# Optimization experiments

Hardware: AMD Instinct MI355X
Metric: run time of the kernel (lower is better)

Reference implementation:

```python
import jax, jax.numpy as jnp
import numpy as np

# ---- static config (from init_kwargs) ----
B_, L_, DM = 4, 2048, 1024
EXPAND, HEADDIM, DSTATE, DCONV = 2, 64, 64, 7
DIN = EXPAND * DM            # 2048
NH = DIN // HEADDIM          # 32
CONV_DIM = DIN + 2 * DSTATE  # 2176 (x, B, C go through the depthwise conv)
DPROJ = 2 * DIN + 2 * DSTATE + 2 * NH  # 4288 (z, xBC, dt_fwd, dt_bwd)
EPS = 1e-5


def setup_inputs() -> dict:
    key = jax.random.key(0)
    ks = jax.random.split(key, 8)
    s = lambda d: 1.0 / np.sqrt(d)
    # dt_bias = inv_softplus(dt) with dt ~ logUniform(1e-3, 0.1)  (Mamba2/Hydra init)
    dt = jnp.exp(jax.random.uniform(ks[3], (NH,)) * (np.log(0.1) - np.log(0.001)) + np.log(0.001))
    return {
        "x": jax.random.normal(ks[0], (B_, L_, DM), jnp.float32),
        "ln_gamma": jnp.ones((DM,), jnp.float32),
        "ln_beta": jnp.zeros((DM,), jnp.float32),
        "W_in": jax.random.normal(ks[1], (DPROJ, DM), jnp.float32) * s(DM),
        "conv_w": jax.random.normal(ks[2], (CONV_DIM, DCONV), jnp.float32) * s(DCONV),
        "conv_b": jnp.zeros((CONV_DIM,), jnp.float32),
        "dt_bias": jnp.log(jnp.expm1(dt)),
        "A_log": jnp.log(jax.random.uniform(ks[4], (NH,), minval=1.0, maxval=16.0)),
        "fc_D_w": jax.random.normal(ks[5], (NH, DIN), jnp.float32) * s(DIN),
        "D": jnp.ones((NH,), jnp.float32),
        "norm_w": jnp.ones((DIN,), jnp.float32),
        "W_out": jax.random.normal(ks[6], (DM, DIN), jnp.float32) * s(DIN),
    }


def _hydra_layer(x, ln_gamma, ln_beta, W_in, conv_w, conv_b, dt_bias, A_log,
                 fc_D_w, D, norm_w, W_out):
    res = x
    # LayerNorm
    mu = jnp.mean(x, -1, keepdims=True)
    var = jnp.mean((x - mu) ** 2, -1, keepdims=True)
    u = (x - mu) * jax.lax.rsqrt(var + EPS) * ln_gamma + ln_beta

    # input projection -> z (gate), xBC (conv stream), dt (fwd+bwd)
    zxbcdt = jnp.einsum('bld,pd->blp', u, W_in)
    z = zxbcdt[..., :DIN]
    xBC = zxbcdt[..., DIN:DIN + CONV_DIM]
    dt = zxbcdt[..., DIN + CONV_DIM:]               # (B,L,2*NH)

    # depthwise 'same' conv along L + SiLU (bidirectional model -> symmetric pad)
    xBC_c = jax.lax.conv_general_dilated(
        xBC.transpose(0, 2, 1), conv_w[:, None, :], (1,),
        [(DCONV // 2, DCONV // 2)], feature_group_count=CONV_DIM)
    xBC = jax.nn.silu((xBC_c + conv_b[None, :, None]).transpose(0, 2, 1))

    xs = xBC[..., :DIN]                             # (B,L,DIN)
    Bm = xBC[..., DIN:DIN + DSTATE]                 # (B,L,N)
    Cm = xBC[..., DIN + DSTATE:]                    # (B,L,N)

    flip = lambda a: a[:, ::-1]
    # stack forward and (flipped) backward direction along batch
    dt2 = jax.nn.softplus(jnp.concatenate([dt[..., :NH], flip(dt[..., NH:])], 0) + dt_bias)  # (2B,L,NH)
    x2 = jnp.concatenate([xs, flip(xs)], 0).reshape(2 * B_, L_, NH, HEADDIM)
    B2 = jnp.concatenate([Bm, flip(Bm)], 0)
    C2 = jnp.concatenate([Cm, flip(Cm)], 0)

    A = -jnp.exp(A_log)                             # (NH,)
    dA = jnp.exp(dt2 * A)                           # (2B,L,NH)

    # selective SSM recurrence: h_t = dA_t * h_{t-1} + dt_t * x_t B_t^T ; y_t = h_t C_t
    def step(h, inp):
        dA_t, dt_t, B_t, C_t, x_t = inp
        dBx = (dt_t[:, :, None, None] * x_t[..., None]) * B_t[:, None, None, :]
        h = dA_t[:, :, None, None] * h + dBx        # (2B,NH,P,N)
        y = jnp.einsum('bhpn,bn->bhp', h, C_t)
        return h, y

    h0 = jnp.zeros((2 * B_, NH, HEADDIM, DSTATE), x.dtype)
    tr = lambda a: jnp.moveaxis(a, 1, 0)
    _, ys = jax.lax.scan(step, h0, (tr(dA), tr(dt2), tr(B2), tr(C2), tr(x2)))
    y = jnp.moveaxis(ys, 0, 1)                      # (2B,L,NH,P)

    # shift by one: strictly off-diagonal part of the quasiseparable mixing matrix
    y = jnp.concatenate([jnp.zeros_like(y[:, :1]), y[:, :-1]], axis=1)
    y = y[:B_] + flip(y[B_:])                       # (B,L,NH,P)

    # data-dependent diagonal: D(x) = fc_D(x) + D, applied per head
    Ddata = jnp.einsum('bld,hd->blh', xs, fc_D_w) + D
    y = y + xs.reshape(B_, L_, NH, HEADDIM) * Ddata[..., None]
    y = y.reshape(B_, L_, DIN)

    # gated RMSNorm (norm after gate)
    y = y * jax.nn.silu(z)
    y = y * jax.lax.rsqrt(jnp.mean(y * y, -1, keepdims=True) + EPS) * norm_w

    # out proj + residual (dropout is identity in eval)
    return res + jnp.einsum('bli,di->bld', y, W_out)


def reference(x, ln_gamma, ln_beta, W_in, conv_w, conv_b, dt_bias, A_log,
              fc_D_w, D, norm_w, W_out):
    return _hydra_layer(x, ln_gamma, ln_beta, W_in, conv_w, conv_b, dt_bias,
                        A_log, fc_D_w, D, norm_w, W_out)
```

## Files before the change

### kernel.cpp

```cpp
#include <hip/hip_runtime.h>
#include <stdint.h>

#define B_   4
#define L_   2048
#define DM   1024
#define DIN  2048
#define NH   32
#define HD   64
#define DSTATE 64
#define DCONV  7
#define CONV_DIM 2176
#define DPROJ 4288
#define NPAD 4352
#define BL   8192
#define EPS  1e-5f
#define QC   128
#define NCH  16

typedef unsigned short u16;
typedef unsigned int   u32;
typedef __bf16 bf16x8 __attribute__((ext_vector_type(8)));
typedef float  f32x4  __attribute__((ext_vector_type(4)));

__device__ __forceinline__ float b2f(u32 b) { return __uint_as_float(b << 16); }
__device__ __forceinline__ u16 f2b(float f) {
    u32 u = __float_as_uint(f);
    u32 r = (u + 0x7fffu + ((u >> 16) & 1u)) >> 16;
    return (u16)r;
}
__device__ __forceinline__ void unpack8(uint4 v, float* f) {
    f[0] = b2f(v.x & 0xffffu); f[1] = b2f(v.x >> 16);
    f[2] = b2f(v.y & 0xffffu); f[3] = b2f(v.y >> 16);
    f[4] = b2f(v.z & 0xffffu); f[5] = b2f(v.z >> 16);
    f[6] = b2f(v.w & 0xffffu); f[7] = b2f(v.w >> 16);
}
__device__ __forceinline__ uint4 pack8(const float* f) {
    uint4 v;
    v.x = (u32)f2b(f[0]) | ((u32)f2b(f[1]) << 16);
    v.y = (u32)f2b(f[2]) | ((u32)f2b(f[3]) << 16);
    v.z = (u32)f2b(f[4]) | ((u32)f2b(f[5]) << 16);
    v.w = (u32)f2b(f[6]) | ((u32)f2b(f[7]) << 16);
    return v;
}
__device__ __forceinline__ int xts(int p, int s) { return p * 136 + ((p >> 3) << 3) + s; }
__device__ __forceinline__ void gload_lds16(const u16* g, u16* l) {
    __builtin_amdgcn_global_load_lds((const __attribute__((address_space(1))) void*)g,
                                     (__attribute__((address_space(3))) void*)l, 16, 0, 0);
}

__global__ __launch_bounds__(256) void k_cvt_win(const float* __restrict__ W, u16* __restrict__ Wb) {
    int idx4 = (blockIdx.x * 256 + threadIdx.x) * 4;
    int n = idx4 >> 10;
    int col = idx4 & 1023;
    uint2 p = {0u, 0u};
    if (n < DPROJ) {
        float4 v = *(const float4*)(W + (size_t)n * DM + col);
        p.x = (u32)f2b(v.x) | ((u32)f2b(v.y) << 16);
        p.y = (u32)f2b(v.z) | ((u32)f2b(v.w) << 16);
    }
    *(uint2*)(Wb + idx4) = p;
}
__global__ __launch_bounds__(256) void k_cvt_wout(const float* __restrict__ W, u16* __restrict__ Wb) {
    int idx4 = (blockIdx.x * 256 + threadIdx.x) * 4;
    float4 v = *(const float4*)(W + idx4);
    uint2 p;
    p.x = (u32)f2b(v.x) | ((u32)f2b(v.y) << 16);
    p.y = (u32)f2b(v.z) | ((u32)f2b(v.w) << 16);
    *(uint2*)(Wb + idx4) = p;
}
__global__ __launch_bounds__(256) void k_cvt_fcd(const float* __restrict__ W, u16* __restrict__ Wb) {
    int idx4 = (blockIdx.x * 256 + threadIdx.x) * 4;
    float4 v = *(const float4*)(W + idx4);
    uint2 p;
    p.x = (u32)f2b(v.x) | ((u32)f2b(v.y) << 16);
    p.y = (u32)f2b(v.z) | ((u32)f2b(v.w) << 16);
    *(uint2*)(Wb + idx4) = p;
}

__global__ __launch_bounds__(256) void k_ln(const float* __restrict__ x, const float* __restrict__ g,
                                            const float* __restrict__ be, u16* __restrict__ u) {
    int row = blockIdx.x, tid = threadIdx.x;
    const float4* xr = (const float4*)(x + (size_t)row * DM);
    float4 v = xr[tid];
    float s1 = v.x + v.y + v.z + v.w;
    float s2 = v.x * v.x + v.y * v.y + v.z * v.z + v.w * v.w;
    for (int o = 32; o; o >>= 1) { s1 += __shfl_down(s1, o); s2 += __shfl_down(s2, o); }
    __shared__ float ls1[4], ls2[4];
    int w = tid >> 6;
    if ((tid & 63) == 0) { ls1[w] = s1; ls2[w] = s2; }
    __syncthreads();
    float t1 = ls1[0] + ls1[1] + ls1[2] + ls1[3];
    float t2 = ls2[0] + ls2[1] + ls2[2] + ls2[3];
    float mu = t1 * (1.f / DM);
    float var = t2 * (1.f / DM) - mu * mu;
    float rs = rsqrtf(var + EPS);
    float4 gv = ((const float4*)g)[tid];
    float4 bv = ((const float4*)be)[tid];
    float o0 = (v.x - mu) * rs * gv.x + bv.x;
    float o1 = (v.y - mu) * rs * gv.y + bv.y;
    float o2 = (v.z - mu) * rs * gv.z + bv.z;
    float o3 = (v.w - mu) * rs * gv.w + bv.w;
    uint2 p;
    p.x = (u32)f2b(o0) | ((u32)f2b(o1) << 16);
    p.y = (u32)f2b(o2) | ((u32)f2b(o3) << 16);
    ((uint2*)(u + (size_t)row * DM))[tid] = p;
}

__global__ __launch_bounds__(256) void k_gemm_bt(const u16* __restrict__ A, const u16* __restrict__ Bw,
                                                 int M, int N, int K, int out_bf16,
                                                 u16* __restrict__ obf, int ldo,
                                                 float* __restrict__ ofp, const float* __restrict__ res) {
    __shared__ __align__(16) u16 As[128 * 64];
    __shared__ __align__(16) u16 Bs[128 * 64];
    int tid = threadIdx.x;
    int m0 = blockIdx.y * 128, n0 = blockIdx.x * 128;
    int w = tid >> 6, lane = tid & 63;
    int wm = (w >> 1) * 64, wn = (w & 1) * 64;
    int lr = lane & 15, lq = lane >> 4;

    f32x4 acc[4][4];
    #pragma unroll
    for (int i = 0; i < 4; i++)
        #pragma unroll
        for (int j = 0; j < 4; j++) acc[i][j] = (f32x4){0.f, 0.f, 0.f, 0.f};

    for (int kt = 0; kt < K; kt += 64) {
        #pragma unroll
        for (int it = 0; it < 4; it++) {
            int s_idx = it * 256 + tid;
            int row = s_idx >> 3;
            int kcg = (s_idx & 7) ^ (row & 7);
            u16* lbase_a = &As[(it * 256 + w * 64) * 8];
            u16* lbase_b = &Bs[(it * 256 + w * 64) * 8];
            gload_lds16(A + (size_t)(m0 + row) * K + kt + kcg * 8, lbase_a);
            gload_lds16(Bw + (size_t)(n0 + row) * K + kt + kcg * 8, lbase_b);
        }
        __syncthreads();
        #pragma unroll
        for (int kk = 0; kk < 2; kk++) {
            bf16x8 af[4], bfr[4];
            #pragma unroll
            for (int i = 0; i < 4; i++) {
                int row = wm + 16 * i + lr;
                af[i] = *(const bf16x8*)&As[row * 64 + (((kk * 4 + lq)) ^ (row & 7)) * 8];
            }
            #pragma unroll
            for (int j = 0; j < 4; j++) {
                int row = wn + 16 * j + lr;
                bfr[j] = *(const bf16x8*)&Bs[row * 64 + (((kk * 4 + lq)) ^ (row & 7)) * 8];
            }
            #pragma unroll
            for (int i = 0; i < 4; i++)
                #pragma unroll
                for (int j = 0; j < 4; j++)
                    acc[i][j] = __builtin_amdgcn_mfma_f32_16x16x32_bf16(af[i], bfr[j], acc[i][j], 0, 0, 0);
        }
        __syncthreads();
    }
    #pragma unroll
    for (int i = 0; i < 4; i++) {
        #pragma unroll
        for (int j = 0; j < 4; j++) {
            #pragma unroll
            for (int rr = 0; rr < 4; rr++) {
                int m = m0 + wm + 16 * i + lq * 4 + rr;
                int n = n0 + wn + 16 * j + lr;
                float v = acc[i][j][rr];
                if (out_bf16) obf[(size_t)m * ldo + n] = f2b(v);
                else          ofp[(size_t)m * ldo + n] = v + res[(size_t)m * ldo + n];
            }
        }
    }
}

__global__ __launch_bounds__(256) void k_dzero(const float* __restrict__ Dv, float* __restrict__ Dd) {
    int idx = blockIdx.x * 256 + threadIdx.x;
    Dd[idx] = Dv[idx & 31];
}

__global__ __launch_bounds__(256) void k_dproj(const u16* __restrict__ xs, const u16* __restrict__ fcb,
                                               float* __restrict__ Dd) {
    __shared__ __align__(16) u16 As[32 * 72];
    __shared__ __align__(16) u16 Bs[32 * 72];
    int tid = threadIdx.x;
    int m0 = blockIdx.x * 32;
    int k0 = blockIdx.y * 256;
    int w = tid >> 6, lane = tid & 63, lr = lane & 15, lq = lane >> 4;
    int mt = (w & 1) * 16, nt = (w >> 1) * 16;
    int r = tid >> 3, kc = tid & 7;
    f32x4 acc = (f32x4){0.f, 0.f, 0.f, 0.f};
    for (int kt = k0; kt < k0 + 256; kt += 64) {
        *(uint4*)&As[r * 72 + kc * 8] = *(const uint4*)(xs + (size_t)(m0 + r) * DIN + kt + kc * 8);
        *(uint4*)&Bs[r * 72 + kc * 8] = *(const uint4*)(fcb + (size_t)r * DIN + kt + kc * 8);
        __syncthreads();
        #pragma unroll
        for (int ks = 0; ks < 2; ks++) {
            bf16x8 a = *(const bf16x8*)&As[(mt + lr) * 72 + ks * 32 + lq * 8];
            bf16x8 b = *(const bf16x8*)&Bs[(nt + lr) * 72 + ks * 32 + lq * 8];
            acc = __builtin_amdgcn_mfma_f32_16x16x32_bf16(a, b, acc, 0, 0, 0);
        }
        __syncthreads();
    }
    #pragma unroll
    for (int rr = 0; rr < 4; rr++) {
        int m = m0 + mt + lq * 4 + rr;
        int n = nt + lr;
        atomicAdd(&Dd[(size_t)m * 32 + n], acc[rr]);
    }
}

__global__ __launch_bounds__(256) void k_conv(const u16* __restrict__ zx, const float* __restrict__ cw,
                                              const float* __restrict__ cb, u16* __restrict__ xs,
                                              u16* __restrict__ BCb) {
    __shared__ u16 sh[262 * 64];
    int c0 = blockIdx.x * 64, t0 = blockIdx.y * 256, b = blockIdx.z;
    int tid = threadIdx.x;
    int c = tid & 63, tg = tid >> 6;
    for (int it = 0; it < 66; it++) {
        int r = it * 4 + tg;
        if (r < 262) {
            int t = t0 + r - 3;
            u16 v = 0;
            if (t >= 0 && t < L_) v = zx[(size_t)(b * L_ + t) * NPAD + DIN + c0 + c];
            sh[r * 64 + c] = v;
        }
    }
    float wgt[7];
    #pragma unroll
    for (int k = 0; k < 7; k++) wgt[k] = cw[(c0 + c) * 7 + k];
    float bias = cb[c0 + c];
    __syncthreads();
    int cg = c0 + c;
    for (int tt = 0; tt < 64; tt++) {
        int tl = tt * 4 + tg;
        float a = bias;
        #pragma unroll
        for (int k = 0; k < 7; k++) a += b2f(sh[(tl + k) * 64 + c]) * wgt[k];
        float v = a / (1.f + __expf(-a));
        size_t row = (size_t)b * L_ + (t0 + tl);
        if (cg < DIN) xs[row * DIN + cg] = f2b(v);
        else          BCb[row * 128 + (cg - DIN)] = f2b(v);
    }
}

__global__ __launch_bounds__(256) void k_chunk(const u16* __restrict__ xs, const u16* __restrict__ BCb,
                                               const u16* __restrict__ zx, const float* __restrict__ dt_bias,
                                               const float* __restrict__ A_log, u16* __restrict__ y0,
                                               u16* __restrict__ y1, float* __restrict__ wout,
                                               float* __restrict__ decay, u16* __restrict__ scb) {
    __shared__ __align__(16) u16 ab[18432];
    __shared__ __align__(16) u16 XT[8768];
    __shared__ __align__(16) u16 BT[8768];
    __shared__ __align__(16) float dts_s[128];
    __shared__ __align__(16) float lda_s[128];
    __shared__ __align__(16) float wend[128];
    __shared__ __align__(16) double cumd[128];

    const int blk = blockIdx.x;
    const int c = blk & 15, dbh = blk >> 4;
    const int h = dbh & 31, b = (dbh >> 5) & 3, dir = dbh >> 7;
    const int tid = threadIdx.x, w = tid >> 6, lane = tid & 63, lr = lane & 15, lq = lane >> 4;
    const int s0 = c * QC;
    u16* yo = dir ? y1 : y0;

    if (tid < 128) {
        int s = s0 + tid;
        int t = dir ? (L_ - 1 - s) : s;
        float draw = b2f(zx[(size_t)(b * L_ + t) * NPAD + (DIN + CONV_DIM) + dir * 32 + h]);
        float xb = draw + dt_bias[h];
        float dt2 = (xb > 20.f) ? xb : log1pf(__expf(xb));
        dts_s[tid] = dt2;
        lda_s[tid] = -__expf(A_log[h]) * dt2;
    }
    {
        int sl0 = tid >> 3, ng = (tid & 7) * 8;
        #pragma unroll
        for (int it = 0; it < 4; it++) {
            int sl = sl0 + it * 32;
            int s = s0 + sl;
            int t = dir ? (L_ - 1 - s) : s;
            size_t row = (size_t)b * L_ + t;
            const u16* bcr = BCb + row * 128;
            uint4 cv = *(const uint4*)(bcr + 64 + ng);
            *(uint4*)&ab[sl * 72 + ng] = cv;
            uint4 pb = *(const uint4*)(bcr + ng);
            *(uint4*)&ab[9216 + sl * 72 + ng] = pb;
            u16 bh[8] = {(u16)(pb.x & 0xffffu), (u16)(pb.x >> 16), (u16)(pb.y & 0xffffu), (u16)(pb.y >> 16),
                         (u16)(pb.z & 0xffffu), (u16)(pb.z >> 16), (u16)(pb.w & 0xffffu), (u16)(pb.w >> 16)};
            #pragma unroll
            for (int i = 0; i < 8; i++) BT[(ng + i) * 136 + ng + sl] = bh[i];
            uint4 xv = *(const uint4*)(xs + row * DIN + h * 64 + ng);
            u16 xh[8] = {(u16)(xv.x & 0xffffu), (u16)(xv.x >> 16), (u16)(xv.y & 0xffffu), (u16)(xv.y >> 16),
                         (u16)(xv.z & 0xffffu), (u16)(xv.z >> 16), (u16)(xv.w & 0xffffu), (u16)(xv.w >> 16)};
            #pragma unroll
            for (int i = 0; i < 8; i++) XT[(ng + i) * 136 + ng + sl] = xh[i];
        }
    }
    __syncthreads();
    if (w == 0) {
        double v0 = (double)lda_s[lane];
        double v1 = (double)lda_s[64 + lane];
        #pragma unroll
        for (int o = 1; o < 64; o <<= 1) {
            double t0 = __shfl_up(v0, o);
            double t1 = __shfl_up(v1, o);
            if (lane >= o) { v0 += t0; v1 += t1; }
        }
        double tot0 = __shfl(v0, 63);
        cumd[lane] = v0;
        cumd[64 + lane] = tot0 + v1;
    }
    bf16x8 af[2][2];
    #pragma unroll
    for (int ti = 0; ti < 2; ti++)
        #pragma unroll
        for (int ks = 0; ks < 2; ks++)
            af[ti][ks] = *(const bf16x8*)&ab[(w * 32 + ti * 16 + lr) * 72 + ks * 32 + lq * 8];
    f32x4 accg[2][8];
    #pragma unroll
    for (int ti = 0; ti < 2; ti++)
        #pragma unroll
        for (int si = 0; si < 8; si++) accg[ti][si] = (f32x4){0.f, 0.f, 0.f, 0.f};
    #pragma unroll
    for (int si = 0; si < 8; si++)
        #pragma unroll
        for (int ks = 0; ks < 2; ks++) {
            bf16x8 bf = *(const bf16x8*)&ab[9216 + (si * 16 + lr) * 72 + ks * 32 + lq * 8];
            accg[0][si] = __builtin_amdgcn_mfma_f32_16x16x32_bf16(af[0][ks], bf, accg[0][si], 0, 0, 0);
            accg[1][si] = __builtin_amdgcn_mfma_f32_16x16x32_bf16(af[1][ks], bf, accg[1][si], 0, 0, 0);
        }
    __syncthreads();
    if (tid < 128) wend[tid] = __expf((float)(cumd[127] - cumd[tid])) * dts_s[tid];
    {
        double cumt_d[8];
        #pragma unroll
        for (int ti = 0; ti < 2; ti++)
            #pragma unroll
            for (int r = 0; r < 4; r++) cumt_d[ti * 4 + r] = cumd[w * 32 + ti * 16 + lq * 4 + r];
        double cums_d[8]; float dts_l[8];
        #pragma unroll
        for (int si = 0; si < 8; si++) { cums_d[si] = cumd[si * 16 + lr]; dts_l[si] = dts_s[si * 16 + lr]; }
        #pragma unroll
        for (int ti = 0; ti < 2; ti++)
            #pragma unroll
            for (int si = 0; si < 8; si++)
                #pragma unroll
                for (int r = 0; r < 4; r++) {
                    int t_l = w * 32 + ti * 16 + lq * 4 + r;
                    int s_l = si * 16 + lr;
                    float v = 0.f;
                    if (s_l <= t_l)
                        v = __expf((float)(cumt_d[ti * 4 + r] - cums_d[si])) * dts_l[si] * accg[ti][si][r];
                    ab[xts(t_l, s_l)] = f2b(v);
                }
    }
    __syncthreads();
    f32x4 acc[2][4];
    #pragma unroll
    for (int ti = 0; ti < 2; ti++)
        #pragma unroll
        for (int pj = 0; pj < 4; pj++) acc[ti][pj] = (f32x4){0.f, 0.f, 0.f, 0.f};
    #pragma unroll
    for (int ks = 0; ks < 4; ks++) {
        bf16x8 a0 = *(const bf16x8*)&ab[xts(w * 32 + lr, ks * 32 + lq * 8)];
        bf16x8 a1 = *(const bf16x8*)&ab[xts(w * 32 + 16 + lr, ks * 32 + lq * 8)];
        #pragma unroll
        for (int pj = 0; pj < 4; pj++) {
            bf16x8 bf = *(const bf16x8*)&XT[xts(pj * 16 + lr, ks * 32 + lq * 8)];
            acc[0][pj] = __builtin_amdgcn_mfma_f32_16x16x32_bf16(a0, bf, acc[0][pj], 0, 0, 0);
            acc[1][pj] = __builtin_amdgcn_mfma_f32_16x16x32_bf16(a1, bf, acc[1][pj], 0, 0, 0);
        }
    }
    f32x4 accs[4];
    #pragma unroll
    for (int nj = 0; nj < 4; nj++) accs[nj] = (f32x4){0.f, 0.f, 0.f, 0.f};
    #pragma unroll
    for (int ks = 0; ks < 4; ks++) {
        uint4 xv = *(const uint4*)&XT[xts(w * 16 + lr, ks * 32 + lq * 8)];
        float xf[8]; unpack8(xv, xf);
        float4 w0 = *(const float4*)&wend[ks * 32 + lq * 8];
        float4 w1 = *(const float4*)&wend[ks * 32 + lq * 8 + 4];
        float fs[8] = {xf[0]*w0.x, xf[1]*w0.y, xf[2]*w0.z, xf[3]*w0.w,
                       xf[4]*w1.x, xf[5]*w1.y, xf[6]*w1.z, xf[7]*w1.w};
        bf16x8 a = __builtin_bit_cast(bf16x8, pack8(fs));
        #pragma unroll
        for (int nj = 0; nj < 4; nj++) {
            bf16x8 bb = *(const bf16x8*)&BT[xts(nj * 16 + lr, ks * 32 + lq * 8)];
            accs[nj] = __builtin_amdgcn_mfma_f32_16x16x32_bf16(a, bb, accs[nj], 0, 0, 0);
        }
    }
    __syncthreads();
    #pragma unroll
    for (int ti = 0; ti < 2; ti++)
        #pragma unroll
        for (int pj = 0; pj < 4; pj++)
            #pragma unroll
            for (int r = 0; r < 4; r++) {
                int t_l = w * 32 + ti * 16 + lq * 4 + r;
                ab[t_l * 72 + pj * 16 + lr] = f2b(acc[ti][pj][r]);
            }
    #pragma unroll
    for (int nj = 0; nj < 4; nj++)
        #pragma unroll
        for (int r = 0; r < 4; r++) {
            int p = w * 16 + lq * 4 + r, n = nj * 16 + lr;
            BT[p * 72 + n] = f2b(accs[nj][r]);
        }
    __syncthreads();
    #pragma unroll
    for (int k2 = 0; k2 < 4; k2++) {
        int c2 = k2 * 256 + tid;
        int t_l = c2 >> 3, p0 = (c2 & 7) * 8;
        int s = s0 + t_l;
        int t = dir ? (L_ - 1 - s) : s;
        *(uint4*)(yo + ((size_t)b * L_ + t) * DIN + h * 64 + p0) = *(const uint4*)&ab[t_l * 72 + p0];
    }
    #pragma unroll
    for (int k2 = 0; k2 < 2; k2++) {
        int c2 = k2 * 256 + tid;
        int p = c2 >> 3, n0 = (c2 & 7) * 8;
        *(uint4*)(scb + (size_t)blk * 4096 + p * 64 + n0) = *(const uint4*)&BT[p * 72 + n0];
    }
    if (tid < 128) wout[dbh * 2048 + s0 + tid] = __expf((float)cumd[tid]);
    if (tid == 0)  decay[blk] = __expf((float)cumd[127]);
}

__global__ __launch_bounds__(256) void k_hscan(const float* __restrict__ decay, u16* __restrict__ scb) {
    int bid = blockIdx.x;
    int dbh = bid >> 2, ps = bid & 3;
    int tid = threadIdx.x;
    u16* base = scb + (size_t)dbh * 16 * 4096 + ps * 1024 + tid * 4;
    float h0 = 0.f, h1 = 0.f, h2 = 0.f, h3 = 0.f;
    for (int c = 0; c < NCH; c++) {
        u16* sg = base + (size_t)c * 4096;
        uint2 q = *(const uint2*)sg;
        float s0 = b2f(q.x & 0xffffu), s1 = b2f(q.x >> 16);
        float s2 = b2f(q.y & 0xffffu), s3 = b2f(q.y >> 16);
        uint2 o;
        o.x = (u32)f2b(h0) | ((u32)f2b(h1) << 16);
        o.y = (u32)f2b(h2) | ((u32)f2b(h3) << 16);
        *(uint2*)sg = o;
        float dk = decay[dbh * 16 + c];
        h0 = dk * h0 + s0; h1 = dk * h1 + s1;
        h2 = dk * h2 + s2; h3 = dk * h3 + s3;
    }
}

__global__ __launch_bounds__(256) void k_inter(const u16* __restrict__ BCb, const float* __restrict__ wout,
                                               const u16* __restrict__ hin, u16* __restrict__ y0,
                                               u16* __restrict__ y1) {
    __shared__ __align__(16) u16 smem[18432];
    u16* Csc = smem;
    u16* hs  = smem + 9216;
    float* fsm = (float*)smem;
    const int blk = blockIdx.x;
    const int c = blk & 15, dbh = blk >> 4;
    const int h = dbh & 31, b = (dbh >> 5) & 3, dir = dbh >> 7;
    const int tid = threadIdx.x, w = tid >> 6, lane = tid & 63, lr = lane & 15, lq = lane >> 4;
    u16* yo = dir ? y1 : y0;

    {
        int g = tid * 16, p = g >> 6, n = g & 63;
        const u16* hg = hin + (size_t)blk * 4096 + g;
        *(uint4*)&hs[p * 72 + n]     = *(const uint4*)hg;
        *(uint4*)&hs[p * 72 + n + 8] = *(const uint4*)(hg + 8);
    }
    const int sl0 = tid >> 3, ng = (tid & 7) * 8;
    #pragma unroll
    for (int it = 0; it < 4; it++) {
        int sl = sl0 + it * 32;
        int s = c * QC + sl;
        int t = dir ? (L_ - 1 - s) : s;
        const u16* bcr = BCb + ((size_t)b * L_ + t) * 128 + 64 + ng;
        float sc = wout[dbh * 2048 + s];
        uint4 cv = *(const uint4*)bcr;
        float cf[8]; unpack8(cv, cf);
        float f[8] = {cf[0]*sc, cf[1]*sc, cf[2]*sc, cf[3]*sc, cf[4]*sc, cf[5]*sc, cf[6]*sc, cf[7]*sc};
        *(uint4*)&Csc[sl * 72 + ng] = pack8(f);
    }
    __syncthreads();
    f32x4 acc[2][4];
    #pragma unroll
    for (int ti = 0; ti < 2; ti++)
        #pragma unroll
        for (int pj = 0; pj < 4; pj++) acc[ti][pj] = (f32x4){0.f, 0.f, 0.f, 0.f};
    #pragma unroll
    for (int ks = 0; ks < 2; ks++) {
        bf16x8 a0 = *(const bf16x8*)&Csc[(w * 32 + lr) * 72 + ks * 32 + lq * 8];
        bf16x8 a1 = *(const bf16x8*)&Csc[(w * 32 + 16 + lr) * 72 + ks * 32 + lq * 8];
        #pragma unroll
        for (int pj = 0; pj < 4; pj++) {
            bf16x8 bb = *(const bf16x8*)&hs[(pj * 16 + lr) * 72 + ks * 32 + lq * 8];
            acc[0][pj] = __builtin_amdgcn_mfma_f32_16x16x32_bf16(a0, bb, acc[0][pj], 0, 0, 0);
            acc[1][pj] = __builtin_amdgcn_mfma_f32_16x16x32_bf16(a1, bb, acc[1][pj], 0, 0, 0);
        }
    }
    __syncthreads();
    #pragma unroll
    for (int ti = 0; ti < 2; ti++)
        #pragma unroll
        for (int pj = 0; pj < 4; pj++)
            #pragma unroll
            for (int r = 0; r < 4; r++) {
                int t_l = w * 32 + ti * 16 + lq * 4 + r;
                fsm[t_l * 68 + pj * 16 + lr] = acc[ti][pj][r];
            }
    __syncthreads();
    #pragma unroll
    for (int k2 = 0; k2 < 4; k2++) {
        int c2 = k2 * 256 + tid;
        int t_l = c2 >> 3, p0 = (c2 & 7) * 8;
        int s = c * QC + t_l;
        int t = dir ? (L_ - 1 - s) : s;
        u16* yp = yo + ((size_t)b * L_ + t) * DIN + h * 64 + p0;
        uint4 ov = *(const uint4*)yp;
        float of[8]; unpack8(ov, of);
        const float4 v0 = *(const float4*)&fsm[t_l * 68 + p0];
        const float4 v1 = *(const float4*)&fsm[t_l * 68 + p0 + 4];
        float nf[8] = {of[0] + v0.x, of[1] + v0.y, of[2] + v0.z, of[3] + v0.w,
                       of[4] + v1.x, of[5] + v1.y, of[6] + v1.z, of[7] + v1.w};
        *(uint4*)yp = pack8(nf);
    }
}

__global__ __launch_bounds__(256) void k_gate(const u16* __restrict__ xs, const u16* __restrict__ zx,
                                              const u16* __restrict__ y0, const u16* __restrict__ y1,
                                              const float* __restrict__ Dd,
                                              const float* __restrict__ nw, u16* __restrict__ yn) {
    int row = blockIdx.x, tid = threadIdx.x;
    int t = row & (L_ - 1);
    __shared__ float red[4];
    size_t base = (size_t)row * DIN;
    uint4 xv = ((const uint4*)(xs + base))[tid];
    uint4 zv = ((const uint4*)(zx + (size_t)row * NPAD))[tid];
    uint4 zero4 = {0u, 0u, 0u, 0u};
    uint4 a0 = (t > 0)      ? ((const uint4*)(y0 + base - DIN))[tid] : zero4;
    uint4 a1 = (t < L_ - 1) ? ((const uint4*)(y1 + base + DIN))[tid] : zero4;
    float sD = Dd[(size_t)row * 32 + (tid >> 3)];
    float xf[8], zf[8], f0[8], f1[8];
    unpack8(xv, xf); unpack8(zv, zf); unpack8(a0, f0); unpack8(a1, f1);
    int d0 = tid * 8;
    float g[8]; float ss = 0.f;
    #pragma unroll
    for (int i = 0; i < 8; i++) {
        float yv = f0[i] + f1[i] + xf[i] * sD;
        float z = zf[i];
        float gg = yv * (z / (1.f + __expf(-z)));
        g[i] = gg; ss += gg * gg;
    }
    for (int o = 32; o; o >>= 1) ss += __shfl_down(ss, o);
    if ((tid & 63) == 0) red[tid >> 6] = ss;
    __syncthreads();
    float tot = red[0] + red[1] + red[2] + red[3];
    float r = rsqrtf(tot * (1.f / DIN) + EPS);
    float o8[8];
    #pragma unroll
    for (int i = 0; i < 8; i++) o8[i] = g[i] * r * nw[d0 + i];
    ((uint4*)(yn + base))[tid] = pack8(o8);
}

#define OFF_U     ((size_t)0)
#define OFF_WIN   ((size_t)16777216)
#define OFF_WOUT  ((size_t)25690112)
#define OFF_ZX    ((size_t)29884416)
#define OFF_XS    ((size_t)101187584)
#define OFF_BC    ((size_t)134742016)
#define OFF_DTA   ((size_t)138936320)
#define OFF_Y0    ((size_t)143130624)
#define OFF_Y1    ((size_t)176685056)
#define OFF_YN    ((size_t)210239488)
#define OFF_WO2   OFF_U
#define OFF_DEC   (OFF_U + 2097152)
#define OFF_FCB   (OFF_U + 2113536)
#define OFF_DD    (OFF_U + 2244608)
#define OFF_SCB   OFF_YN

extern "C" void kernel_launch(void* const* d_in, const int* in_sizes, int n_in,
                              void* d_out, int out_size, void* d_ws, size_t ws_size,
                              hipStream_t stream) {
    const float* x       = (const float*)d_in[0];
    const float* ln_g    = (const float*)d_in[1];
    const float* ln_b    = (const float*)d_in[2];
    const float* W_in    = (const float*)d_in[3];
    const float* conv_w  = (const float*)d_in[4];
    const float* conv_b  = (const float*)d_in[5];
    const float* dt_bias = (const float*)d_in[6];
    const float* A_log   = (const float*)d_in[7];
    const float* fc_D_w  = (const float*)d_in[8];
    const float* Dv      = (const float*)d_in[9];
    const float* norm_w  = (const float*)d_in[10];
    const float* W_out   = (const float*)d_in[11];

    char* ws = (char*)d_ws;
    u16*   u_bf  = (u16*)(ws + OFF_U);
    u16*   winb  = (u16*)(ws + OFF_WIN);
    u16*   woutb = (u16*)(ws + OFF_WOUT);
    u16*   zx    = (u16*)(ws + OFF_ZX);
    u16*   xs    = (u16*)(ws + OFF_XS);
    u16*   BCb   = (u16*)(ws + OFF_BC);
    u16*   y0b   = (u16*)(ws + OFF_Y0);
    u16*   y1b   = (u16*)(ws + OFF_Y1);
    u16*   ynb   = (u16*)(ws + OFF_YN);
    float* wo2   = (float*)(ws + OFF_WO2);
    float* dec   = (float*)(ws + OFF_DEC);
    u16*   fcb   = (u16*)(ws + OFF_FCB);
    float* Dd    = (float*)(ws + OFF_DD);
    u16*   scb   = (u16*)(ws + OFF_SCB);

    k_cvt_win <<<(NPAD * DM) / 1024, 256, 0, stream>>>(W_in, winb);
    k_cvt_wout<<<(DM * DIN) / 1024, 256, 0, stream>>>(W_out, woutb);
    k_ln      <<<BL, 256, 0, stream>>>(x, ln_g, ln_b, u_bf);
    k_gemm_bt <<<dim3(NPAD / 128, BL / 128), 256, 0, stream>>>(u_bf, winb, BL, NPAD, DM, 1, zx, NPAD, nullptr, nullptr);
    k_cvt_fcd <<<(NH * DIN) / 1024, 256, 0, stream>>>(fc_D_w, fcb);
    k_dzero   <<<(BL * 32) / 256, 256, 0, stream>>>(Dv, Dd);
    k_conv    <<<dim3(CONV_DIM / 64, L_ / 256, B_), 256, 0, stream>>>(zx, conv_w, conv_b, xs, BCb);
    k_dproj   <<<dim3(BL / 32, 8), 256, 0, stream>>>(xs, fcb, Dd);
    k_chunk   <<<4096, 256, 0, stream>>>(xs, BCb, zx, dt_bias, A_log, y0b, y1b, wo2, dec, scb);
    k_hscan   <<<1024, 256, 0, stream>>>(dec, scb);
    k_inter   <<<4096, 256, 0, stream>>>(BCb, wo2, scb, y0b, y1b);
    k_gate    <<<BL, 256, 0, stream>>>(xs, zx, y0b, y1b, Dd, norm_w, ynb);
    k_gemm_bt <<<dim3(DM / 128, BL / 128), 256, 0, stream>>>(ynb, woutb, BL, DM, DIN, 0, nullptr, DM, (float*)d_out, x);
}
```

Before: 519.3 us.

## Fuse inter-chunk state scan into inter-chunk output kernel; merge prep kernels

Merges the sequential chunk-state scan (k_hscan) with the inter-chunk C·h contribution (k_inter) into one kernel. Each block owns a 16-wide slice of headdim, keeps the running state in registers and walks all 16 chunks in order, so the scanned states are never written back to global memory and one launch is dropped. The LayerNorm and weight-conversion launches are also merged into two combined prep kernels to cut launch overhead. In exchange the grid shrinks from 4096 to 1024 blocks with a serial 16-chunk loop, which lowers parallelism. The C tile is also reloaded and rescaled per block, so this work is repeated four times per head.

After: 546.7 us. 5.3% more time.

```diff
diff --git a/kernel.cpp b/kernel.cpp
--- a/kernel.cpp
+++ b/kernel.cpp
@@ -48,62 +48,76 @@
                                      (__attribute__((address_space(3))) void*)l, 16, 0, 0);
 }
 
-__global__ __launch_bounds__(256) void k_cvt_win(const float* __restrict__ W, u16* __restrict__ Wb) {
-    int idx4 = (blockIdx.x * 256 + threadIdx.x) * 4;
-    int n = idx4 >> 10;
-    int col = idx4 & 1023;
-    uint2 p = {0u, 0u};
-    if (n < DPROJ) {
-        float4 v = *(const float4*)(W + (size_t)n * DM + col);
+#define GP_LN    8192
+#define GP_WIN   4352
+#define GP_WOUT  2048
+#define GP_FCD   64
+#define GP_DZ    1024
+__global__ __launch_bounds__(256) void k_prep_a(const float* __restrict__ x, const float* __restrict__ g,
+                                                const float* __restrict__ be, u16* __restrict__ u,
+                                                const float* __restrict__ Wi, u16* __restrict__ wib,
+                                                const float* __restrict__ Wo, u16* __restrict__ wob) {
+    int bb = blockIdx.x, tid = threadIdx.x;
+    if (bb < GP_LN) {
+        int row = bb;
+        const float4* xr = (const float4*)(x + (size_t)row * DM);
+        float4 v = xr[tid];
+        float s1 = v.x + v.y + v.z + v.w;
+        float s2 = v.x * v.x + v.y * v.y + v.z * v.z + v.w * v.w;
+        for (int o = 32; o; o >>= 1) { s1 += __shfl_down(s1, o); s2 += __shfl_down(s2, o); }
+        __shared__ float ls1[4], ls2[4];
+        int w = tid >> 6;
+        if ((tid & 63) == 0) { ls1[w] = s1; ls2[w] = s2; }
+        __syncthreads();
+        float t1 = ls1[0] + ls1[1] + ls1[2] + ls1[3];
+        float t2 = ls2[0] + ls2[1] + ls2[2] + ls2[3];
+        float mu = t1 * (1.f / DM);
+        float var = t2 * (1.f / DM) - mu * mu;
+        float rs = rsqrtf(var + EPS);
+        float4 gv = ((const float4*)g)[tid];
+        float4 bv = ((const float4*)be)[tid];
+        float o0 = (v.x - mu) * rs * gv.x + bv.x;
+        float o1 = (v.y - mu) * rs * gv.y + bv.y;
+        float o2 = (v.z - mu) * rs * gv.z + bv.z;
+        float o3 = (v.w - mu) * rs * gv.w + bv.w;
+        uint2 p;
+        p.x = (u32)f2b(o0) | ((u32)f2b(o1) << 16);
+        p.y = (u32)f2b(o2) | ((u32)f2b(o3) << 16);
+        ((uint2*)(u + (size_t)row * DM))[tid] = p;
+    } else if (bb < GP_LN + GP_WIN) {
+        int idx4 = ((bb - GP_LN) * 256 + tid) * 4;
+        int n = idx4 >> 10, col = idx4 & 1023;
+        uint2 p = {0u, 0u};
+        if (n < DPROJ) {
+            float4 v = *(const float4*)(Wi + (size_t)n * DM + col);
+            p.x = (u32)f2b(v.x) | ((u32)f2b(v.y) << 16);
+            p.y = (u32)f2b(v.z) | ((u32)f2b(v.w) << 16);
+        }
+        *(uint2*)(wib + idx4) = p;
+    } else {
+        int idx4 = ((bb - GP_LN - GP_WIN) * 256 + tid) * 4;
+        float4 v = *(const float4*)(Wo + idx4);
+        uint2 p;
         p.x = (u32)f2b(v.x) | ((u32)f2b(v.y) << 16);
         p.y = (u32)f2b(v.z) | ((u32)f2b(v.w) << 16);
-    }
-    *(uint2*)(Wb + idx4) = p;
-}
-__global__ __launch_bounds__(256) void k_cvt_wout(const float* __restrict__ W, u16* __restrict__ Wb) {
-    int idx4 = (blockIdx.x * 256 + threadIdx.x) * 4;
-    float4 v = *(const float4*)(W + idx4);
-    uint2 p;
-    p.x = (u32)f2b(v.x) | ((u32)f2b(v.y) << 16);
-    p.y = (u32)f2b(v.z) | ((u32)f2b(v.w) << 16);
-    *(uint2*)(Wb + idx4) = p;
-}
-__global__ __launch_bounds__(256) void k_cvt_fcd(const float* __restrict__ W, u16* __restrict__ Wb) {
-    int idx4 = (blockIdx.x * 256 + threadIdx.x) * 4;
-    float4 v = *(const float4*)(W + idx4);
-    uint2 p;
-    p.x = (u32)f2b(v.x) | ((u32)f2b(v.y) << 16);
-    p.y = (u32)f2b(v.z) | ((u32)f2b(v.w) << 16);
-    *(uint2*)(Wb + idx4) = p;
-}
-
-__global__ __launch_bounds__(256) void k_ln(const float* __restrict__ x, const float* __restrict__ g,
-                                            const float* __restrict__ be, u16* __restrict__ u) {
-    int row = blockIdx.x, tid = threadIdx.x;
-    const float4* xr = (const float4*)(x + (size_t)row * DM);
-    float4 v = xr[tid];
-    float s1 = v.x + v.y + v.z + v.w;
-    float s2 = v.x * v.x + v.y * v.y + v.z * v.z + v.w * v.w;
-    for (int o = 32; o; o >>= 1) { s1 += __shfl_down(s1, o); s2 += __shfl_down(s2, o); }
-    __shared__ float ls1[4], ls2[4];
-    int w = tid >> 6;
-    if ((tid & 63) == 0) { ls1[w] = s1; ls2[w] = s2; }
-    __syncthreads();
-    float t1 = ls1[0] + ls1[1] + ls1[2] + ls1[3];
-    float t2 = ls2[0] + ls2[1] + ls2[2] + ls2[3];
-    float mu = t1 * (1.f / DM);
-    float var = t2 * (1.f / DM) - mu * mu;
-    float rs = rsqrtf(var + EPS);
-    float4 gv = ((const float4*)g)[tid];
-    float4 bv = ((const float4*)be)[tid];
-    float o0 = (v.x - mu) * rs * gv.x + bv.x;
-    float o1 = (v.y - mu) * rs * gv.y + bv.y;
-    float o2 = (v.z - mu) * rs * gv.z + bv.z;
-    float o3 = (v.w - mu) * rs * gv.w + bv.w;
-    uint2 p;
-    p.x = (u32)f2b(o0) | ((u32)f2b(o1) << 16);
-    p.y = (u32)f2b(o2) | ((u32)f2b(o3) << 16);
-    ((uint2*)(u + (size_t)row * DM))[tid] = p;
+        *(uint2*)(wob + idx4) = p;
+    }
+}
+
+__global__ __launch_bounds__(256) void k_prep_b(const float* __restrict__ Wf, u16* __restrict__ fcb,
+                                                const float* __restrict__ Dv, float* __restrict__ Dd) {
+    int bb = blockIdx.x, tid = threadIdx.x;
+    if (bb < GP_FCD) {
+        int idx4 = (bb * 256 + tid) * 4;
+        float4 v = *(const float4*)(Wf + idx4);
+        uint2 p;
+        p.x = (u32)f2b(v.x) | ((u32)f2b(v.y) << 16);
+        p.y = (u32)f2b(v.z) | ((u32)f2b(v.w) << 16);
+        *(uint2*)(fcb + idx4) = p;
+    } else {
+        int idx = (bb - GP_FCD) * 256 + tid;
+        Dd[idx] = Dv[idx & 31];
+    }
 }
 
 __global__ __launch_bounds__(256) void k_gemm_bt(const u16* __restrict__ A, const u16* __restrict__ Bw,
@@ -171,11 +185,6 @@
             }
         }
     }
-}
-
-__global__ __launch_bounds__(256) void k_dzero(const float* __restrict__ Dv, float* __restrict__ Dd) {
-    int idx = blockIdx.x * 256 + threadIdx.x;
-    Dd[idx] = Dv[idx & 31];
 }
 
 __global__ __launch_bounds__(256) void k_dproj(const u16* __restrict__ xs, const u16* __restrict__ fcb,
@@ -425,101 +434,86 @@
     if (tid == 0)  decay[blk] = __expf((float)cumd[127]);
 }
 
-__global__ __launch_bounds__(256) void k_hscan(const float* __restrict__ decay, u16* __restrict__ scb) {
-    int bid = blockIdx.x;
-    int dbh = bid >> 2, ps = bid & 3;
-    int tid = threadIdx.x;
-    u16* base = scb + (size_t)dbh * 16 * 4096 + ps * 1024 + tid * 4;
-    float h0 = 0.f, h1 = 0.f, h2 = 0.f, h3 = 0.f;
-    for (int c = 0; c < NCH; c++) {
-        u16* sg = base + (size_t)c * 4096;
-        uint2 q = *(const uint2*)sg;
-        float s0 = b2f(q.x & 0xffffu), s1 = b2f(q.x >> 16);
-        float s2 = b2f(q.y & 0xffffu), s3 = b2f(q.y >> 16);
-        uint2 o;
-        o.x = (u32)f2b(h0) | ((u32)f2b(h1) << 16);
-        o.y = (u32)f2b(h2) | ((u32)f2b(h3) << 16);
-        *(uint2*)sg = o;
-        float dk = decay[dbh * 16 + c];
-        h0 = dk * h0 + s0; h1 = dk * h1 + s1;
-        h2 = dk * h2 + s2; h3 = dk * h3 + s3;
-    }
-}
-
-__global__ __launch_bounds__(256) void k_inter(const u16* __restrict__ BCb, const float* __restrict__ wout,
-                                               const u16* __restrict__ hin, u16* __restrict__ y0,
-                                               u16* __restrict__ y1) {
-    __shared__ __align__(16) u16 smem[18432];
-    u16* Csc = smem;
-    u16* hs  = smem + 9216;
-    float* fsm = (float*)smem;
-    const int blk = blockIdx.x;
-    const int c = blk & 15, dbh = blk >> 4;
+__global__ __launch_bounds__(256) void k_hinter(const u16* __restrict__ BCb, const float* __restrict__ wout,
+                                                const float* __restrict__ decay, const u16* __restrict__ scb,
+                                                u16* __restrict__ y0, u16* __restrict__ y1) {
+    __shared__ __align__(16) u16 Csc[128 * 72];
+    __shared__ __align__(16) u16 hs[16 * 72];
+    __shared__ __align__(16) float ybuf[128 * 20];
+    const int bid = blockIdx.x;
+    const int dbh = bid >> 2, ps = bid & 3;
+    const int p0 = ps * 16;
     const int h = dbh & 31, b = (dbh >> 5) & 3, dir = dbh >> 7;
     const int tid = threadIdx.x, w = tid >> 6, lane = tid & 63, lr = lane & 15, lq = lane >> 4;
     u16* yo = dir ? y1 : y0;
 
-    {
-        int g = tid * 16, p = g >> 6, n = g & 63;
-        const u16* hg = hin + (size_t)blk * 4096 + g;
-        *(uint4*)&hs[p * 72 + n]     = *(const uint4*)hg;
-        *(uint4*)&hs[p * 72 + n + 8] = *(const uint4*)(hg + 8);
-    }
+    const int hp = tid >> 4;
+    const int hn = (tid & 15) * 4;
+    float hreg[4] = {0.f, 0.f, 0.f, 0.f};
+
     const int sl0 = tid >> 3, ng = (tid & 7) * 8;
-    #pragma unroll
-    for (int it = 0; it < 4; it++) {
-        int sl = sl0 + it * 32;
-        int s = c * QC + sl;
-        int t = dir ? (L_ - 1 - s) : s;
-        const u16* bcr = BCb + ((size_t)b * L_ + t) * 128 + 64 + ng;
-        float sc = wout[dbh * 2048 + s];
-        uint4 cv = *(const uint4*)bcr;
-        float cf[8]; unpack8(cv, cf);
-        float f[8] = {cf[0]*sc, cf[1]*sc, cf[2]*sc, cf[3]*sc, cf[4]*sc, cf[5]*sc, cf[6]*sc, cf[7]*sc};
-        *(uint4*)&Csc[sl * 72 + ng] = pack8(f);
-    }
-    __syncthreads();
-    f32x4 acc[2][4];
-    #pragma unroll
-    for (int ti = 0; ti < 2; ti++)
-        #pragma unroll
-        for (int pj = 0; pj < 4; pj++) acc[ti][pj] = (f32x4){0.f, 0.f, 0.f, 0.f};
-    #pragma unroll
-    for (int ks = 0; ks < 2; ks++) {
-        bf16x8 a0 = *(const bf16x8*)&Csc[(w * 32 + lr) * 72 + ks * 32 + lq * 8];
-        bf16x8 a1 = *(const bf16x8*)&Csc[(w * 32 + 16 + lr) * 72 + ks * 32 + lq * 8];
-        #pragma unroll
-        for (int pj = 0; pj < 4; pj++) {
-            bf16x8 bb = *(const bf16x8*)&hs[(pj * 16 + lr) * 72 + ks * 32 + lq * 8];
-            acc[0][pj] = __builtin_amdgcn_mfma_f32_16x16x32_bf16(a0, bb, acc[0][pj], 0, 0, 0);
-            acc[1][pj] = __builtin_amdgcn_mfma_f32_16x16x32_bf16(a1, bb, acc[1][pj], 0, 0, 0);
-        }
-    }
-    __syncthreads();
-    #pragma unroll
-    for (int ti = 0; ti < 2; ti++)
-        #pragma unroll
-        for (int pj = 0; pj < 4; pj++)
+    const int rmw_t = tid >> 1, rmw_p = (tid & 1) * 8;
+
+    for (int c = 0; c < NCH; c++) {
+        {
+            uint2 pk;
+            pk.x = (u32)f2b(hreg[0]) | ((u32)f2b(hreg[1]) << 16);
+            pk.y = (u32)f2b(hreg[2]) | ((u32)f2b(hreg[3]) << 16);
+            *(uint2*)&hs[hp * 72 + hn] = pk;
+        }
+        #pragma unroll
+        for (int it = 0; it < 4; it++) {
+            int sl = sl0 + it * 32;
+            int s = c * QC + sl;
+            int t = dir ? (L_ - 1 - s) : s;
+            const u16* bcr = BCb + ((size_t)b * L_ + t) * 128 + 64 + ng;
+            float sc = wout[dbh * 2048 + s];
+            uint4 cv = *(const uint4*)bcr;
+            float cf[8]; unpack8(cv, cf);
+            float f[8] = {cf[0]*sc, cf[1]*sc, cf[2]*sc, cf[3]*sc, cf[4]*sc, cf[5]*sc, cf[6]*sc, cf[7]*sc};
+            *(uint4*)&Csc[sl * 72 + ng] = pack8(f);
+        }
+        __syncthreads();
+        f32x4 acc[2];
+        acc[0] = (f32x4){0.f, 0.f, 0.f, 0.f};
+        acc[1] = (f32x4){0.f, 0.f, 0.f, 0.f};
+        #pragma unroll
+        for (int ks = 0; ks < 2; ks++) {
+            bf16x8 a0 = *(const bf16x8*)&Csc[(w * 32 + lr) * 72 + ks * 32 + lq * 8];
+            bf16x8 a1 = *(const bf16x8*)&Csc[(w * 32 + 16 + lr) * 72 + ks * 32 + lq * 8];
+            bf16x8 bb = *(const bf16x8*)&hs[lr * 72 + ks * 32 + lq * 8];
+            acc[0] = __builtin_amdgcn_mfma_f32_16x16x32_bf16(a0, bb, acc[0], 0, 0, 0);
+            acc[1] = __builtin_amdgcn_mfma_f32_16x16x32_bf16(a1, bb, acc[1], 0, 0, 0);
+        }
+        {
+            const u16* sg = scb + (size_t)(dbh * 16 + c) * 4096 + (p0 + hp) * 64 + hn;
+            uint2 q = *(const uint2*)sg;
+            float dk = decay[dbh * 16 + c];
+            hreg[0] = dk * hreg[0] + b2f(q.x & 0xffffu);
+            hreg[1] = dk * hreg[1] + b2f(q.x >> 16);
+            hreg[2] = dk * hreg[2] + b2f(q.y & 0xffffu);
+            hreg[3] = dk * hreg[3] + b2f(q.y >> 16);
+        }
+        #pragma unroll
+        for (int ti = 0; ti < 2; ti++)
             #pragma unroll
             for (int r = 0; r < 4; r++) {
                 int t_l = w * 32 + ti * 16 + lq * 4 + r;
-                fsm[t_l * 68 + pj * 16 + lr] = acc[ti][pj][r];
+                ybuf[t_l * 20 + lr] = acc[ti][r];
             }
-    __syncthreads();
-    #pragma unroll
-    for (int k2 = 0; k2 < 4; k2++) {
-        int c2 = k2 * 256 + tid;
-        int t_l = c2 >> 3, p0 = (c2 & 7) * 8;
-        int s = c * QC + t_l;
-        int t = dir ? (L_ - 1 - s) : s;
-        u16* yp = yo + ((size_t)b * L_ + t) * DIN + h * 64 + p0;
-        uint4 ov = *(const uint4*)yp;
-        float of[8]; unpack8(ov, of);
-        const float4 v0 = *(const float4*)&fsm[t_l * 68 + p0];
-        const float4 v1 = *(const float4*)&fsm[t_l * 68 + p0 + 4];
-        float nf[8] = {of[0] + v0.x, of[1] + v0.y, of[2] + v0.z, of[3] + v0.w,
-                       of[4] + v1.x, of[5] + v1.y, of[6] + v1.z, of[7] + v1.w};
-        *(uint4*)yp = pack8(nf);
+        __syncthreads();
+        {
+            int s = c * QC + rmw_t;
+            int t = dir ? (L_ - 1 - s) : s;
+            u16* yp = yo + ((size_t)b * L_ + t) * DIN + h * 64 + p0 + rmw_p;
+            uint4 ov = *(const uint4*)yp;
+            float of[8]; unpack8(ov, of);
+            float nf[8];
+            #pragma unroll
+            for (int i = 0; i < 8; i++) nf[i] = of[i] + ybuf[rmw_t * 20 + rmw_p + i];
+            *(uint4*)yp = pack8(nf);
+        }
+        __syncthreads();
     }
 }
 
@@ -607,17 +601,14 @@
     float* Dd    = (float*)(ws + OFF_DD);
     u16*   scb   = (u16*)(ws + OFF_SCB);
 
-    k_cvt_win <<<(NPAD * DM) / 1024, 256, 0, stream>>>(W_in, winb);
-    k_cvt_wout<<<(DM * DIN) / 1024, 256, 0, stream>>>(W_out, woutb);
-    k_ln      <<<BL, 256, 0, stream>>>(x, ln_g, ln_b, u_bf);
+    k_prep_a  <<<GP_LN + GP_WIN + GP_WOUT, 256, 0, stream>>>
+              (x, ln_g, ln_b, u_bf, W_in, winb, W_out, woutb);
     k_gemm_bt <<<dim3(NPAD / 128, BL / 128), 256, 0, stream>>>(u_bf, winb, BL, NPAD, DM, 1, zx, NPAD, nullptr, nullptr);
-    k_cvt_fcd <<<(NH * DIN) / 1024, 256, 0, stream>>>(fc_D_w, fcb);
-    k_dzero   <<<(BL * 32) / 256, 256, 0, stream>>>(Dv, Dd);
+    k_prep_b  <<<GP_FCD + GP_DZ, 256, 0, stream>>>(fc_D_w, fcb, Dv, Dd);
     k_conv    <<<dim3(CONV_DIM / 64, L_ / 256, B_), 256, 0, stream>>>(zx, conv_w, conv_b, xs, BCb);
     k_dproj   <<<dim3(BL / 32, 8), 256, 0, stream>>>(xs, fcb, Dd);
     k_chunk   <<<4096, 256, 0, stream>>>(xs, BCb, zx, dt_bias, A_log, y0b, y1b, wo2, dec, scb);
-    k_hscan   <<<1024, 256, 0, stream>>>(dec, scb);
-    k_inter   <<<4096, 256, 0, stream>>>(BCb, wo2, scb, y0b, y1b);
+    k_hinter  <<<1024, 256, 0, stream>>>(BCb, wo2, dec, scb, y0b, y1b);
     k_gate    <<<BL, 256, 0, stream>>>(xs, zx, y0b, y1b, Dd, norm_w, ynb);
     k_gemm_bt <<<dim3(DM / 128, BL / 128), 256, 0, stream>>>(ynb, woutb, BL, DM, DIN, 0, nullptr, DM, (float*)d_out, x);
 }
```
